# Optimization experiments

Hardware: AMD Instinct MI355X
Metric: run time of the kernel (lower is better)

## Reference

```python
import jax, jax.numpy as jnp
import numpy as np

B, D, H, C, T, F = 4096, 1024, 2048, 1000, 819200, 32


def setup_inputs() -> dict:
    key = jax.random.key(0)
    ks = jax.random.split(key, 12)
    feature_vector = jax.random.normal(ks[0], (B, D), dtype=jnp.float32)
    var_flat = jax.random.normal(ks[1], (T, F), dtype=jnp.float32)
    segment_ids = jnp.sort(jax.random.randint(ks[2], (T,), 0, B))
    target_vector = jax.random.randint(ks[3], (B,), 0, C)
    target_scalar = jax.random.normal(ks[4], (B,), dtype=jnp.float32)
    # learned params (torch Linear convention: W [out, in])
    Wv = jax.random.normal(ks[5], (D, F), dtype=jnp.float32) / np.sqrt(F)
    bv = jnp.zeros((D,), dtype=jnp.float32)
    W1 = jax.random.normal(ks[6], (H, D), dtype=jnp.float32) / np.sqrt(D)
    b1 = jnp.zeros((H,), dtype=jnp.float32)
    W2 = jax.random.normal(ks[7], (C, H), dtype=jnp.float32) / np.sqrt(H)
    b2 = jnp.zeros((C,), dtype=jnp.float32)
    Ws = jax.random.normal(ks[8], (1, H), dtype=jnp.float32) / np.sqrt(H)
    bs = jnp.zeros((1,), dtype=jnp.float32)
    return {
        "feature_vector": feature_vector, "var_flat": var_flat,
        "segment_ids": segment_ids, "target_vector": target_vector,
        "target_scalar": target_scalar, "Wv": Wv, "bv": bv,
        "W1": W1, "b1": b1, "W2": W2, "b2": b2, "Ws": Ws, "bs": bs,
    }


def reference(feature_vector, var_flat, segment_ids, target_vector, target_scalar,
              Wv, bv, W1, b1, W2, b2, Ws, bs):
    nb = feature_vector.shape[0]
    # ragged per-item mean via segment reduce (replaces python loop)
    sums = jax.ops.segment_sum(var_flat, segment_ids, num_segments=nb)      # [B, 32]
    counts = jax.ops.segment_sum(jnp.ones((var_flat.shape[0],), var_flat.dtype),
                                 segment_ids, num_segments=nb)
    means = sums / jnp.maximum(counts, 1.0)[:, None]
    var_processed = means @ Wv.T + bv                                        # [B, D]
    combined = feature_vector + var_processed
    hidden = jax.nn.relu(combined @ W1.T + b1)                               # [B, H]
    vector_output = hidden @ W2.T + b2                                       # [B, C]
    scalar_output = (hidden @ Ws.T + bs).squeeze(-1)                         # [B]
    logp = jax.nn.log_softmax(vector_output, axis=-1)
    loss_vector = -jnp.mean(jnp.take_along_axis(logp, target_vector[:, None], axis=1))
    loss_scalar = jnp.mean(jnp.square(scalar_output - target_scalar))
    total_loss = loss_vector + loss_scalar
    acc = jnp.mean((jnp.argmax(vector_output, axis=1) == target_vector).astype(jnp.float32))
    return total_loss, loss_vector, loss_scalar, acc
```

## Files before the change

### kernel.cpp

```cpp
#include <hip/hip_runtime.h>
#include <hip/hip_bf16.h>
#include <math.h>

#define B_  4096
#define D_  1024
#define H_  2048
#define C_  1000
#define T_  819200
#define F_  32
#define NPAD2 1024
#define NPART 1024

typedef __attribute__((ext_vector_type(8))) short short8;
typedef __attribute__((ext_vector_type(4))) float f32x4;

static const size_t WS_SUMS     = 0;
static const size_t WS_COUNTS   = WS_SUMS + (size_t)B_ * F_ * 4;
static const size_t WS_ZERO_SZ  = WS_COUNTS + (size_t)B_ * 4;
static const size_t WS_PV       = WS_ZERO_SZ;
static const size_t WS_PA       = WS_PV + NPART * 4;
static const size_t WS_PS       = WS_PA + NPART * 4;
static const size_t WS_B2P      = WS_PS + NPART * 4;
static const size_t WS_COMBINED = 1u << 20;
static const size_t WS_W1BF     = WS_COMBINED + (size_t)B_ * D_ * 2;
static const size_t WS_W2BF     = WS_W1BF + (size_t)H_ * D_ * 2;
static const size_t WS_HIDDEN   = WS_W2BF + (size_t)NPAD2 * H_ * 2;
static const size_t WS_LOGITS   = WS_HIDDEN + (size_t)B_ * H_ * 2;

#define RPT 32
__global__ __launch_bounds__(256) void seg_reduce_kernel(
    const float* __restrict__ var_flat, const int* __restrict__ seg_ids,
    float* __restrict__ sums, float* __restrict__ counts) {
  int gt  = blockIdx.x * 256 + threadIdx.x;
  int c4  = (gt & 7) * 4;
  long base = (long)(gt >> 3) * RPT;
  int cur = -1;
  float a0 = 0.f, a1 = 0.f, a2 = 0.f, a3 = 0.f, cnt = 0.f;
#define FLUSH_SEG()                                              \
  if (cur >= 0) {                                                \
    float* dst = &sums[(size_t)cur * F_ + c4];                   \
    atomicAdd(dst + 0, a0); atomicAdd(dst + 1, a1);              \
    atomicAdd(dst + 2, a2); atomicAdd(dst + 3, a3);              \
    if (c4 == 0) atomicAdd(&counts[cur], cnt);                   \
    a0 = a1 = a2 = a3 = 0.f; cnt = 0.f;                          \
  }
  for (int rr = 0; rr < RPT; rr += 8) {
    int4 sa = *(const int4*)(seg_ids + base + rr);
    int4 sb = *(const int4*)(seg_ids + base + rr + 4);
    float4 v[8];
#pragma unroll
    for (int e = 0; e < 8; ++e)
      v[e] = *(const float4*)(var_flat + (base + rr + e) * F_ + c4);
    int s[8] = {sa.x, sa.y, sa.z, sa.w, sb.x, sb.y, sb.z, sb.w};
    if (s[0] == s[7]) {
      if (s[0] != cur) { FLUSH_SEG(); cur = s[0]; }
#pragma unroll
      for (int e = 0; e < 8; ++e) {
        a0 += v[e].x; a1 += v[e].y; a2 += v[e].z; a3 += v[e].w;
      }
      cnt += 8.f;
    } else {
#pragma unroll
      for (int e = 0; e < 8; ++e) {
        if (s[e] != cur) { FLUSH_SEG(); cur = s[e]; }
        a0 += v[e].x; a1 += v[e].y; a2 += v[e].z; a3 += v[e].w; cnt += 1.f;
      }
    }
  }
  FLUSH_SEG();
#undef FLUSH_SEG
}

__global__ __launch_bounds__(256) void cvt_bf16_kernel(
    const float* __restrict__ src, __hip_bfloat16* __restrict__ dst, int n8) {
  int i = blockIdx.x * 256 + threadIdx.x;
  if (i >= n8) return;
  size_t off = (size_t)i * 8;
  float4 a = *(const float4*)(src + off);
  float4 b = *(const float4*)(src + off + 4);
  __hip_bfloat16 t[8];
  t[0] = __float2bfloat16(a.x); t[1] = __float2bfloat16(a.y);
  t[2] = __float2bfloat16(a.z); t[3] = __float2bfloat16(a.w);
  t[4] = __float2bfloat16(b.x); t[5] = __float2bfloat16(b.y);
  t[6] = __float2bfloat16(b.z); t[7] = __float2bfloat16(b.w);
  *(uint4*)(dst + off) = *(uint4*)t;
}

__global__ __launch_bounds__(256) void cvt_w2_kernel(
    const float* __restrict__ W2, const float* __restrict__ Ws,
    __hip_bfloat16* __restrict__ dst) {
  int i = blockIdx.x * 256 + threadIdx.x;
  size_t off = (size_t)i * 8;
  int row = (int)(off / H_);
  __hip_bfloat16 t[8];
  const float* src = nullptr;
  if (row < C_)       src = W2 + off;
  else if (row == C_) src = Ws + (off - (size_t)C_ * H_);
  if (src) {
    float4 a = *(const float4*)(src);
    float4 b = *(const float4*)(src + 4);
    t[0] = __float2bfloat16(a.x); t[1] = __float2bfloat16(a.y);
    t[2] = __float2bfloat16(a.z); t[3] = __float2bfloat16(a.w);
    t[4] = __float2bfloat16(b.x); t[5] = __float2bfloat16(b.y);
    t[6] = __float2bfloat16(b.z); t[7] = __float2bfloat16(b.w);
  } else {
    for (int e = 0; e < 8; ++e) t[e] = __float2bfloat16(0.f);
  }
  *(uint4*)(dst + off) = *(uint4*)t;
}

__global__ __launch_bounds__(256) void pad_bias_kernel(
    const float* __restrict__ b2, const float* __restrict__ bs,
    float* __restrict__ b2p) {
  int i = blockIdx.x * 256 + threadIdx.x;
  float v = 0.f;
  if (i < C_) v = b2[i];
  else if (i == C_) v = bs[0];
  b2p[i] = v;
}

__global__ __launch_bounds__(256) void combined_kernel(
    const float* __restrict__ feat, const float* __restrict__ sums,
    const float* __restrict__ counts, const float* __restrict__ Wv,
    const float* __restrict__ bv, __hip_bfloat16* __restrict__ combined) {
  __shared__ float m[8][F_];
  int b0  = blockIdx.y * 8;
  int tid = threadIdx.x;
  {
    int seg = tid >> 5, col = tid & 31;
    float c = counts[b0 + seg];
    c = c < 1.f ? 1.f : c;
    m[seg][col] = sums[(size_t)(b0 + seg) * F_ + col] / c;
  }
  __syncthreads();
  int d = blockIdx.x * 256 + tid;
  float w[F_];
  {
    const float4* wv = (const float4*)(Wv + (size_t)d * F_);
#pragma unroll
    for (int f4 = 0; f4 < F_ / 4; ++f4) {
      float4 x = wv[f4];
      w[f4 * 4 + 0] = x.x; w[f4 * 4 + 1] = x.y;
      w[f4 * 4 + 2] = x.z; w[f4 * 4 + 3] = x.w;
    }
  }
  float bvd = bv[d];
#pragma unroll
  for (int bb = 0; bb < 8; ++bb) {
    float acc = feat[(size_t)(b0 + bb) * D_ + d] + bvd;
#pragma unroll
    for (int f = 0; f < F_; ++f) acc = fmaf(m[bb][f], w[f], acc);
    combined[(size_t)(b0 + bb) * D_ + d] = __float2bfloat16(acc);
  }
}

__device__ inline void load16_lds(const short* g, short* l) {
  __builtin_amdgcn_global_load_lds(
      (const __attribute__((address_space(1))) void*)g,
      (__attribute__((address_space(3))) void*)l, 16, 0, 0);
}

template <int MODE>
__global__ __launch_bounds__(256) void gemm_mfma_kernel(
    const short* __restrict__ A, const short* __restrict__ Bm,
    const float* __restrict__ bias, void* __restrict__ Cout,
    int M, int K, int Nout) {
  __shared__ short As[2][2048];
  __shared__ short Bs[2][4096];
  const int tid  = threadIdx.x;
  const int lane = tid & 63;
  const int w    = tid >> 6;
  const int bm = blockIdx.y * 64;
  const int bn = blockIdx.x * 128;
  const int wm = (w >> 1) * 32;
  const int wn = (w & 1) * 64;
  const int m_lane = lane & 15;
  const int quad   = lane >> 4;

  f32x4 acc[2][4];
#pragma unroll
  for (int i = 0; i < 2; ++i)
#pragma unroll
    for (int j = 0; j < 4; ++j) acc[i][j] = f32x4{0.f, 0.f, 0.f, 0.f};

  const short* gA = A + (size_t)(bm + lane) * K + w * 8;
  const int cb0 = w * 128 + lane;
  const int cb1 = cb0 + 64;
  const short* gB0 = Bm + (size_t)(bn + (cb0 & 127)) * K + w * 8;
  const short* gB1 = Bm + (size_t)(bn + (cb1 & 127)) * K + w * 8;
  const int lA = w * 512;
  const int lB0 = w * 1024;
  const int lB1 = lB0 + 512;

  load16_lds(gA,  &As[0][lA]);
  load16_lds(gB0, &Bs[0][lB0]);
  load16_lds(gB1, &Bs[0][lB1]);

  const int iters = K >> 5;
  for (int it = 0; it < iters; ++it) {
    const int cur = it & 1, nxt = cur ^ 1;
    __syncthreads();
    const int k1 = (it + 1) << 5;
    if (k1 < K) {
      load16_lds(gA + k1,  &As[nxt][lA]);
      load16_lds(gB0 + k1, &Bs[nxt][lB0]);
      load16_lds(gB1 + k1, &Bs[nxt][lB1]);
    }
    short8 af[2], bf[4];
#pragma unroll
    for (int i = 0; i < 2; ++i)
      af[i] = *(const short8*)&As[cur][quad * 512 + (wm + i * 16 + m_lane) * 8];
#pragma unroll
    for (int j = 0; j < 4; ++j)
      bf[j] = *(const short8*)&Bs[cur][quad * 1024 + (wn + j * 16 + m_lane) * 8];
#pragma unroll
    for (int i = 0; i < 2; ++i)
#pragma unroll
      for (int j = 0; j < 4; ++j)
        acc[i][j] = __builtin_amdgcn_mfma_f32_16x16x32_bf16(af[i], bf[j], acc[i][j], 0, 0, 0);
  }

  const int row0 = bm + wm + quad * 4;
  const int col0 = bn + wn + m_lane;
  if (MODE == 0) {
    __hip_bfloat16* Cb = (__hip_bfloat16*)Cout;
#pragma unroll
    for (int j = 0; j < 4; ++j) {
      int col = col0 + j * 16;
      float bsv = bias[col];
#pragma unroll
      for (int i = 0; i < 2; ++i)
#pragma unroll
        for (int r = 0; r < 4; ++r) {
          int row = row0 + i * 16 + r;
          float v = acc[i][j][r] + bsv;
          v = v > 0.f ? v : 0.f;
          Cb[(size_t)row * Nout + col] = __float2bfloat16(v);
        }
    }
  } else {
    float* Cf = (float*)Cout;
#pragma unroll
    for (int j = 0; j < 4; ++j) {
      int col = col0 + j * 16;
      float bsv = bias[col];
#pragma unroll
      for (int i = 0; i < 2; ++i)
#pragma unroll
        for (int r = 0; r < 4; ++r) {
          int row = row0 + i * 16 + r;
          Cf[(size_t)row * Nout + col] = acc[i][j][r] + bsv;
        }
    }
  }
}

__global__ __launch_bounds__(256) void loss_kernel(
    const float* __restrict__ logits, const int* __restrict__ target,
    const float* __restrict__ tgt_scal,
    float* __restrict__ pv, float* __restrict__ pa, float* __restrict__ ps) {
  int tid  = threadIdx.x;
  int lane = tid & 63;
  int w    = tid >> 6;
  int b    = blockIdx.x * 4 + w;
  const float*  row  = logits + (size_t)b * NPAD2;
  const float4* row4 = (const float4*)row;
  float v[16];
  float vmax = -INFINITY;
  int   imax = 0x7fffffff;
#pragma unroll
  for (int k = 0; k < 4; ++k) {
    int c4 = lane + 64 * k;
    float4 x = row4[c4];
    float e0 = x.x, e1 = x.y, e2 = x.z, e3 = x.w;
    int idx = c4 * 4;
    if (idx + 0 >= C_) e0 = -INFINITY;
    if (idx + 1 >= C_) e1 = -INFINITY;
    if (idx + 2 >= C_) e2 = -INFINITY;
    if (idx + 3 >= C_) e3 = -INFINITY;
    v[k * 4 + 0] = e0; v[k * 4 + 1] = e1; v[k * 4 + 2] = e2; v[k * 4 + 3] = e3;
    if (e0 > vmax) { vmax = e0; imax = idx + 0; }
    if (e1 > vmax) { vmax = e1; imax = idx + 1; }
    if (e2 > vmax) { vmax = e2; imax = idx + 2; }
    if (e3 > vmax) { vmax = e3; imax = idx + 3; }
  }
#pragma unroll
  for (int o = 32; o > 0; o >>= 1) {
    float ov = __shfl_down(vmax, o, 64);
    int   oi = __shfl_down(imax, o, 64);
    if (ov > vmax || (ov == vmax && oi < imax)) { vmax = ov; imax = oi; }
  }
  vmax = __shfl(vmax, 0, 64);
  float se = 0.f;
#pragma unroll
  for (int j = 0; j < 16; ++j) se += expf(v[j] - vmax);
#pragma unroll
  for (int o = 32; o > 0; o >>= 1) se += __shfl_down(se, o, 64);
  __shared__ float s_nll[4], s_acc[4], s_sq[4];
  if (lane == 0) {
    int t = target[b];
    float logp = row[t] - vmax - logf(se);
    s_nll[w] = -logp;
    s_acc[w] = (imax == t) ? 1.f : 0.f;
    float d = row[C_] - tgt_scal[b];
    s_sq[w] = d * d;
  }
  __syncthreads();
  if (tid == 0) {
    pv[blockIdx.x] = s_nll[0] + s_nll[1] + s_nll[2] + s_nll[3];
    pa[blockIdx.x] = s_acc[0] + s_acc[1] + s_acc[2] + s_acc[3];
    ps[blockIdx.x] = s_sq[0] + s_sq[1] + s_sq[2] + s_sq[3];
  }
}

__global__ __launch_bounds__(256) void finalize_kernel(
    const float* __restrict__ pv, const float* __restrict__ pa,
    const float* __restrict__ ps, float* __restrict__ out) {
  int tid  = threadIdx.x;
  int lane = tid & 63;
  int w    = tid >> 6;
  float nll = 0.f, acc = 0.f, sq = 0.f;
  for (int i = tid; i < NPART; i += 256) {
    nll += pv[i]; acc += pa[i]; sq += ps[i];
  }
#pragma unroll
  for (int o = 32; o > 0; o >>= 1) {
    nll += __shfl_down(nll, o, 64);
    acc += __shfl_down(acc, o, 64);
    sq  += __shfl_down(sq,  o, 64);
  }
  __shared__ float sn[4], sa[4], ss[4];
  if (lane == 0) { sn[w] = nll; sa[w] = acc; ss[w] = sq; }
  __syncthreads();
  if (tid == 0) {
    float lv = (sn[0] + sn[1] + sn[2] + sn[3]) * (1.f / B_);
    float ls = (ss[0] + ss[1] + ss[2] + ss[3]) * (1.f / B_);
    float ac = (sa[0] + sa[1] + sa[2] + sa[3]) * (1.f / B_);
    out[0] = lv + ls;
    out[1] = lv;
    out[2] = ls;
    out[3] = ac;
  }
}

extern "C" void kernel_launch(void* const* d_in, const int* in_sizes, int n_in,
                              void* d_out, int out_size, void* d_ws, size_t ws_size,
                              hipStream_t stream) {
  const float* feature  = (const float*)d_in[0];
  const float* var_flat = (const float*)d_in[1];
  const int*   seg_ids  = (const int*)d_in[2];
  const int*   tgt_vec  = (const int*)d_in[3];
  const float* tgt_scal = (const float*)d_in[4];
  const float* Wv = (const float*)d_in[5];
  const float* bv = (const float*)d_in[6];
  const float* W1 = (const float*)d_in[7];
  const float* b1 = (const float*)d_in[8];
  const float* W2 = (const float*)d_in[9];
  const float* b2 = (const float*)d_in[10];
  const float* Ws = (const float*)d_in[11];
  const float* bs = (const float*)d_in[12];
  float* out = (float*)d_out;

  char* ws = (char*)d_ws;
  float* sums   = (float*)(ws + WS_SUMS);
  float* counts = (float*)(ws + WS_COUNTS);
  float* pv     = (float*)(ws + WS_PV);
  float* pa     = (float*)(ws + WS_PA);
  float* ps     = (float*)(ws + WS_PS);
  float* b2p    = (float*)(ws + WS_B2P);
  __hip_bfloat16* combined_bf = (__hip_bfloat16*)(ws + WS_COMBINED);
  __hip_bfloat16* W1bf        = (__hip_bfloat16*)(ws + WS_W1BF);
  __hip_bfloat16* W2bf        = (__hip_bfloat16*)(ws + WS_W2BF);
  __hip_bfloat16* hidden_bf   = (__hip_bfloat16*)(ws + WS_HIDDEN);
  float*          logits      = (float*)(ws + WS_LOGITS);

  hipMemsetAsync(ws, 0, WS_ZERO_SZ, stream);

  seg_reduce_kernel<<<(T_ / RPT) * 8 / 256, 256, 0, stream>>>(var_flat, seg_ids, sums, counts);

  cvt_bf16_kernel<<<(H_ * D_ / 8 + 255) / 256, 256, 0, stream>>>(W1, W1bf, H_ * D_ / 8);
  cvt_w2_kernel<<<(NPAD2 * H_ / 8) / 256, 256, 0, stream>>>(W2, Ws, W2bf);
  pad_bias_kernel<<<NPAD2 / 256, 256, 0, stream>>>(b2, bs, b2p);

  {
    dim3 grid(D_ / 256, B_ / 8);
    combined_kernel<<<grid, 256, 0, stream>>>(feature, sums, counts, Wv, bv, combined_bf);
  }

  {
    dim3 grid(H_ / 128, B_ / 64);
    gemm_mfma_kernel<0><<<grid, 256, 0, stream>>>(
        (const short*)combined_bf, (const short*)W1bf, b1, hidden_bf, B_, D_, H_);
  }

  {
    dim3 grid(NPAD2 / 128, B_ / 64);
    gemm_mfma_kernel<1><<<grid, 256, 0, stream>>>(
        (const short*)hidden_bf, (const short*)W2bf, b2p, logits, B_, H_, NPAD2);
  }

  loss_kernel<<<B_ / 4, 256, 0, stream>>>(logits, tgt_vec, tgt_scal, pv, pa, ps);

  finalize_kernel<<<1, 256, 0, stream>>>(pv, pa, ps, out);
}
```

Baseline: 340.3 us.

## Store GEMM operands in k-octet-major layout for coalesced LDS-direct loads

```diff
diff --git a/kernel.cpp b/kernel.cpp
--- a/kernel.cpp
+++ b/kernel.cpp
@@ -71,42 +71,47 @@
 #undef FLUSH_SEG
 }
 
-__global__ __launch_bounds__(256) void cvt_bf16_kernel(
-    const float* __restrict__ src, __hip_bfloat16* __restrict__ dst, int n8) {
-  int i = blockIdx.x * 256 + threadIdx.x;
-  if (i >= n8) return;
-  size_t off = (size_t)i * 8;
-  float4 a = *(const float4*)(src + off);
-  float4 b = *(const float4*)(src + off + 4);
+__global__ __launch_bounds__(256) void cvt_w1_oct_kernel(
+    const float* __restrict__ W1, __hip_bfloat16* __restrict__ dst) {
+  int tid = threadIdx.x;
+  int d0 = blockIdx.x * 64;
+  int n0 = blockIdx.y * 32;
+  int n_l = tid >> 3, kc = tid & 7;
+  int n = n0 + n_l;
+  int dd = d0 + kc * 8;
+  float4 a = *(const float4*)(W1 + (size_t)n * D_ + dd);
+  float4 b = *(const float4*)(W1 + (size_t)n * D_ + dd + 4);
   __hip_bfloat16 t[8];
   t[0] = __float2bfloat16(a.x); t[1] = __float2bfloat16(a.y);
   t[2] = __float2bfloat16(a.z); t[3] = __float2bfloat16(a.w);
   t[4] = __float2bfloat16(b.x); t[5] = __float2bfloat16(b.y);
   t[6] = __float2bfloat16(b.z); t[7] = __float2bfloat16(b.w);
-  *(uint4*)(dst + off) = *(uint4*)t;
-}
-
-__global__ __launch_bounds__(256) void cvt_w2_kernel(
+  *(uint4*)(dst + ((size_t)(blockIdx.x * 8 + kc) * H_ + n) * 8) = *(uint4*)t;
+}
+
+__global__ __launch_bounds__(256) void cvt_w2_oct_kernel(
     const float* __restrict__ W2, const float* __restrict__ Ws,
     __hip_bfloat16* __restrict__ dst) {
-  int i = blockIdx.x * 256 + threadIdx.x;
-  size_t off = (size_t)i * 8;
-  int row = (int)(off / H_);
-  __hip_bfloat16 t[8];
+  int tid = threadIdx.x;
+  int h0 = blockIdx.x * 64;
+  int n0 = blockIdx.y * 32;
+  int n_l = tid >> 3, kc = tid & 7;
+  int n = n0 + n_l;
+  int hh = h0 + kc * 8;
+  float va[8] = {0.f, 0.f, 0.f, 0.f, 0.f, 0.f, 0.f, 0.f};
   const float* src = nullptr;
-  if (row < C_)       src = W2 + off;
-  else if (row == C_) src = Ws + (off - (size_t)C_ * H_);
+  if (n < C_)       src = W2 + (size_t)n * H_ + hh;
+  else if (n == C_) src = Ws + hh;
   if (src) {
     float4 a = *(const float4*)(src);
     float4 b = *(const float4*)(src + 4);
-    t[0] = __float2bfloat16(a.x); t[1] = __float2bfloat16(a.y);
-    t[2] = __float2bfloat16(a.z); t[3] = __float2bfloat16(a.w);
-    t[4] = __float2bfloat16(b.x); t[5] = __float2bfloat16(b.y);
-    t[6] = __float2bfloat16(b.z); t[7] = __float2bfloat16(b.w);
-  } else {
-    for (int e = 0; e < 8; ++e) t[e] = __float2bfloat16(0.f);
-  }
-  *(uint4*)(dst + off) = *(uint4*)t;
+    va[0] = a.x; va[1] = a.y; va[2] = a.z; va[3] = a.w;
+    va[4] = b.x; va[5] = b.y; va[6] = b.z; va[7] = b.w;
+  }
+  __hip_bfloat16 t[8];
+#pragma unroll
+  for (int e = 0; e < 8; ++e) t[e] = __float2bfloat16(va[e]);
+  *(uint4*)(dst + ((size_t)(blockIdx.x * 8 + kc) * NPAD2 + n) * 8) = *(uint4*)t;
 }
 
 __global__ __launch_bounds__(256) void pad_bias_kernel(
@@ -122,36 +127,47 @@
 __global__ __launch_bounds__(256) void combined_kernel(
     const float* __restrict__ feat, const float* __restrict__ sums,
     const float* __restrict__ counts, const float* __restrict__ Wv,
-    const float* __restrict__ bv, __hip_bfloat16* __restrict__ combined) {
-  __shared__ float m[8][F_];
-  int b0  = blockIdx.y * 8;
+    const float* __restrict__ bv, __hip_bfloat16* __restrict__ comb_oct) {
+  __shared__ float m_s[32][F_ + 1];
+  __shared__ float wv_s[64][F_ + 1];
   int tid = threadIdx.x;
-  {
-    int seg = tid >> 5, col = tid & 31;
-    float c = counts[b0 + seg];
+  int d0 = blockIdx.x * 64;
+  int b0 = blockIdx.y * 32;
+  {
+    int b_l = tid >> 3, f4 = (tid & 7) * 4;
+    float c = counts[b0 + b_l];
     c = c < 1.f ? 1.f : c;
-    m[seg][col] = sums[(size_t)(b0 + seg) * F_ + col] / c;
+    float4 s4 = *(const float4*)(sums + (size_t)(b0 + b_l) * F_ + f4);
+    m_s[b_l][f4 + 0] = s4.x / c; m_s[b_l][f4 + 1] = s4.y / c;
+    m_s[b_l][f4 + 2] = s4.z / c; m_s[b_l][f4 + 3] = s4.w / c;
+  }
+  {
+    int r = tid >> 2, p = (tid & 3) * 8;
+    float4 a = *(const float4*)(Wv + (size_t)(d0 + r) * F_ + p);
+    float4 b = *(const float4*)(Wv + (size_t)(d0 + r) * F_ + p + 4);
+    wv_s[r][p + 0] = a.x; wv_s[r][p + 1] = a.y; wv_s[r][p + 2] = a.z; wv_s[r][p + 3] = a.w;
+    wv_s[r][p + 4] = b.x; wv_s[r][p + 5] = b.y; wv_s[r][p + 6] = b.z; wv_s[r][p + 7] = b.w;
   }
   __syncthreads();
-  int d = blockIdx.x * 256 + tid;
-  float w[F_];
-  {
-    const float4* wv = (const float4*)(Wv + (size_t)d * F_);
-#pragma unroll
-    for (int f4 = 0; f4 < F_ / 4; ++f4) {
-      float4 x = wv[f4];
-      w[f4 * 4 + 0] = x.x; w[f4 * 4 + 1] = x.y;
-      w[f4 * 4 + 2] = x.z; w[f4 * 4 + 3] = x.w;
-    }
-  }
-  float bvd = bv[d];
-#pragma unroll
-  for (int bb = 0; bb < 8; ++bb) {
-    float acc = feat[(size_t)(b0 + bb) * D_ + d] + bvd;
-#pragma unroll
-    for (int f = 0; f < F_; ++f) acc = fmaf(m[bb][f], w[f], acc);
-    combined[(size_t)(b0 + bb) * D_ + d] = __float2bfloat16(acc);
-  }
+  int b_l = tid >> 3, kc = tid & 7;
+  int b = b0 + b_l;
+  int dbase = d0 + kc * 8;
+  float4 f0 = *(const float4*)(feat + (size_t)b * D_ + dbase);
+  float4 f1 = *(const float4*)(feat + (size_t)b * D_ + dbase + 4);
+  float4 v0 = *(const float4*)(bv + dbase);
+  float4 v1 = *(const float4*)(bv + dbase + 4);
+  float fv[8]  = {f0.x, f0.y, f0.z, f0.w, f1.x, f1.y, f1.z, f1.w};
+  float bvv[8] = {v0.x, v0.y, v0.z, v0.w, v1.x, v1.y, v1.z, v1.w};
+  __hip_bfloat16 outv[8];
+#pragma unroll
+  for (int e = 0; e < 8; ++e) {
+    float acc = fv[e] + bvv[e];
+    const float* wr = wv_s[kc * 8 + e];
+#pragma unroll
+    for (int f = 0; f < F_; ++f) acc = fmaf(m_s[b_l][f], wr[f], acc);
+    outv[e] = __float2bfloat16(acc);
+  }
+  *(uint4*)(comb_oct + ((size_t)(blockIdx.x * 8 + kc) * B_ + b) * 8) = *(uint4*)outv;
 }
 
 __device__ inline void load16_lds(const short* g, short* l) {
@@ -164,7 +180,7 @@
 __global__ __launch_bounds__(256) void gemm_mfma_kernel(
     const short* __restrict__ A, const short* __restrict__ Bm,
     const float* __restrict__ bias, void* __restrict__ Cout,
-    int M, int K, int Nout) {
+    int M, int Nrows, int K, int Nout) {
   __shared__ short As[2][2048];
   __shared__ short Bs[2][4096];
   const int tid  = threadIdx.x;
@@ -183,12 +199,12 @@
 #pragma unroll
     for (int j = 0; j < 4; ++j) acc[i][j] = f32x4{0.f, 0.f, 0.f, 0.f};
 
-  const short* gA = A + (size_t)(bm + lane) * K + w * 8;
-  const int cb0 = w * 128 + lane;
-  const int cb1 = cb0 + 64;
-  const short* gB0 = Bm + (size_t)(bn + (cb0 & 127)) * K + w * 8;
-  const short* gB1 = Bm + (size_t)(bn + (cb1 & 127)) * K + w * 8;
-  const int lA = w * 512;
+  const size_t strideA = (size_t)M * 32;
+  const size_t strideB = (size_t)Nrows * 32;
+  const short* gA  = A  + ((size_t)w * M + bm) * 8 + lane * 8;
+  const short* gB0 = Bm + ((size_t)w * Nrows + bn) * 8 + lane * 8;
+  const short* gB1 = gB0 + 64 * 8;
+  const int lA  = w * 512;
   const int lB0 = w * 1024;
   const int lB1 = lB0 + 512;
 
@@ -200,11 +216,11 @@
   for (int it = 0; it < iters; ++it) {
     const int cur = it & 1, nxt = cur ^ 1;
     __syncthreads();
-    const int k1 = (it + 1) << 5;
-    if (k1 < K) {
-      load16_lds(gA + k1,  &As[nxt][lA]);
-      load16_lds(gB0 + k1, &Bs[nxt][lB0]);
-      load16_lds(gB1 + k1, &Bs[nxt][lB1]);
+    if (it + 1 < iters) {
+      load16_lds(gA + strideA,  &As[nxt][lA]);
+      load16_lds(gB0 + strideB, &Bs[nxt][lB0]);
+      load16_lds(gB1 + strideB, &Bs[nxt][lB1]);
+      gA += strideA; gB0 += strideB; gB1 += strideB;
     }
     short8 af[2], bf[4];
 #pragma unroll
@@ -228,6 +244,7 @@
     for (int j = 0; j < 4; ++j) {
       int col = col0 + j * 16;
       float bsv = bias[col];
+      __hip_bfloat16* base = Cb + ((size_t)(col >> 3) * M) * 8 + (col & 7);
 #pragma unroll
       for (int i = 0; i < 2; ++i)
 #pragma unroll
@@ -235,7 +252,7 @@
           int row = row0 + i * 16 + r;
           float v = acc[i][j][r] + bsv;
           v = v > 0.f ? v : 0.f;
-          Cb[(size_t)row * Nout + col] = __float2bfloat16(v);
+          base[(size_t)row * 8] = __float2bfloat16(v);
         }
     }
   } else {
@@ -368,35 +385,39 @@
   float* pa     = (float*)(ws + WS_PA);
   float* ps     = (float*)(ws + WS_PS);
   float* b2p    = (float*)(ws + WS_B2P);
-  __hip_bfloat16* combined_bf = (__hip_bfloat16*)(ws + WS_COMBINED);
-  __hip_bfloat16* W1bf        = (__hip_bfloat16*)(ws + WS_W1BF);
-  __hip_bfloat16* W2bf        = (__hip_bfloat16*)(ws + WS_W2BF);
-  __hip_bfloat16* hidden_bf   = (__hip_bfloat16*)(ws + WS_HIDDEN);
-  float*          logits      = (float*)(ws + WS_LOGITS);
+  __hip_bfloat16* comb_oct = (__hip_bfloat16*)(ws + WS_COMBINED);
+  __hip_bfloat16* W1oct    = (__hip_bfloat16*)(ws + WS_W1BF);
+  __hip_bfloat16* W2oct    = (__hip_bfloat16*)(ws + WS_W2BF);
+  __hip_bfloat16* hid_oct  = (__hip_bfloat16*)(ws + WS_HIDDEN);
+  float*          logits   = (float*)(ws + WS_LOGITS);
 
   hipMemsetAsync(ws, 0, WS_ZERO_SZ, stream);
 
   seg_reduce_kernel<<<(T_ / RPT) * 8 / 256, 256, 0, stream>>>(var_flat, seg_ids, sums, counts);
 
-  cvt_bf16_kernel<<<(H_ * D_ / 8 + 255) / 256, 256, 0, stream>>>(W1, W1bf, H_ * D_ / 8);
-  cvt_w2_kernel<<<(NPAD2 * H_ / 8) / 256, 256, 0, stream>>>(W2, Ws, W2bf);
-  pad_bias_kernel<<<NPAD2 / 256, 256, 0, stream>>>(b2, bs, b2p);
-
-  {
-    dim3 grid(D_ / 256, B_ / 8);
-    combined_kernel<<<grid, 256, 0, stream>>>(feature, sums, counts, Wv, bv, combined_bf);
+  {
+    dim3 g1(D_ / 64, H_ / 32);
+    cvt_w1_oct_kernel<<<g1, 256, 0, stream>>>(W1, W1oct);
+    dim3 g2(H_ / 64, NPAD2 / 32);
+    cvt_w2_oct_kernel<<<g2, 256, 0, stream>>>(W2, Ws, W2oct);
+    pad_bias_kernel<<<NPAD2 / 256, 256, 0, stream>>>(b2, bs, b2p);
+  }
+
+  {
+    dim3 grid(D_ / 64, B_ / 32);
+    combined_kernel<<<grid, 256, 0, stream>>>(feature, sums, counts, Wv, bv, comb_oct);
   }
 
   {
     dim3 grid(H_ / 128, B_ / 64);
     gemm_mfma_kernel<0><<<grid, 256, 0, stream>>>(
-        (const short*)combined_bf, (const short*)W1bf, b1, hidden_bf, B_, D_, H_);
+        (const short*)comb_oct, (const short*)W1oct, b1, hid_oct, B_, H_, D_, H_);
   }
 
   {
     dim3 grid(NPAD2 / 128, B_ / 64);
     gemm_mfma_kernel<1><<<grid, 256, 0, stream>>>(
-        (const short*)hidden_bf, (const short*)W2bf, b2p, logits, B_, H_, NPAD2);
+        (const short*)hid_oct, (const short*)W2oct, b2p, logits, B_, NPAD2, H_, NPAD2);
   }
 
   loss_kernel<<<B_ / 4, 256, 0, stream>>>(logits, tgt_vec, tgt_scal, pv, pa, ps);
```

Measured after the change: 295.3 us. -13.2%, faster.
